# Optimization experiments

Hardware: AMD Instinct MI355X
Metric: run time of the kernel (lower is better)

## Reference

```python
import jax, jax.numpy as jnp
import numpy as np

N = 50000        # nodes
E = 800000       # edges
E_PAIR = 200000  # pos/neg link pairs
IN = 256
HID = (512, 256, 160)
NEG_SLOPE = 0.2


def _lin_w(k, i, o):
    s = 1.0 / np.sqrt(i)
    return jax.random.uniform(k, (i, o), jnp.float32, -s, s)


def setup_inputs() -> dict:
    key = jax.random.key(0)
    ks = jax.random.split(key, 16)
    inp = {
        'x': jax.random.normal(ks[0], (N, IN), jnp.float32),
        'w': jax.random.uniform(ks[1], (E,), jnp.float32),
        'src': jax.random.randint(ks[2], (E,), 0, N),
        'dst': jax.random.randint(ks[3], (E,), 0, N),
        'pos_src': jax.random.randint(ks[4], (E_PAIR,), 0, N),
        'pos_dst': jax.random.randint(ks[5], (E_PAIR,), 0, N),
        'neg_src': jax.random.randint(ks[6], (E_PAIR,), 0, N),
        'neg_dst': jax.random.randint(ks[7], (E_PAIR,), 0, N),
        # GraphConv weights/biases
        'W1': _lin_w(ks[8], IN, HID[0]), 'b1': jnp.zeros((HID[0],), jnp.float32),
        'W2': _lin_w(ks[9], HID[0], HID[1]), 'b2': jnp.zeros((HID[1],), jnp.float32),
        'W3': _lin_w(ks[10], HID[1], HID[2]), 'b3': jnp.zeros((HID[2],), jnp.float32),
        # predictor MLP: 160 -> 80 -> 40 -> 1
        'P1': _lin_w(ks[11], HID[2], HID[2] // 2), 'pb1': jnp.zeros((HID[2] // 2,), jnp.float32),
        'P2': _lin_w(ks[12], HID[2] // 2, HID[2] // 4), 'pb2': jnp.zeros((HID[2] // 4,), jnp.float32),
        'P3': _lin_w(ks[13], HID[2] // 4, 1), 'pb3': jnp.zeros((1,), jnp.float32),
    }
    return inp


def _degree_norms(src, dst):
    ones = jnp.ones((E,), jnp.float32)
    out_deg = jnp.clip(jax.ops.segment_sum(ones, src, num_segments=N), 1.0)
    in_deg = jnp.clip(jax.ops.segment_sum(ones, dst, num_segments=N), 1.0)
    # norm='both': D_out^{-1/2} on source side, D_in^{-1/2} on dest side
    return (out_deg ** -0.5)[:, None], (in_deg ** -0.5)[:, None]


def _graph_conv(h, W, b, src, dst, w, out_norm, in_norm, project_first):
    # DGL GraphConv (norm='both', edge_weight=w): scale src feats, multiply
    # messages by edge weight, sum-aggregate, scale by in-degree norm, + bias.
    # DGL projects before aggregation iff in_feats > out_feats (same math).
    h = h * out_norm
    if project_first:
        h = h @ W
    agg = jax.ops.segment_sum(h[src] * w[:, None], dst, num_segments=N)
    if not project_first:
        agg = agg @ W
    return agg * in_norm + b


def _predictor(z, P1, pb1, P2, pb2, P3, pb3):
    z = jax.nn.leaky_relu(z @ P1 + pb1, NEG_SLOPE)
    z = jax.nn.leaky_relu(z @ P2 + pb2, NEG_SLOPE)
    return z @ P3 + pb3


def reference(x, w, src, dst, pos_src, pos_dst, neg_src, neg_dst,
              W1, b1, W2, b2, W3, b3, P1, pb1, P2, pb2, P3, pb3):
    out_norm, in_norm = _degree_norms(src, dst)
    h = _graph_conv(x, W1, b1, src, dst, w, out_norm, in_norm, project_first=False)  # 256<=512
    h = jax.nn.relu(h)
    h = _graph_conv(h, W2, b2, src, dst, w, out_norm, in_norm, project_first=True)   # 512>256
    h = jax.nn.relu(h)
    h = _graph_conv(h, W3, b3, src, dst, w, out_norm, in_norm, project_first=True)   # 256>160
    h_pos = _predictor(h[pos_src] * h[pos_dst], P1, pb1, P2, pb2, P3, pb3)
    h_neg = _predictor(h[neg_src] * h[neg_dst], P1, pb1, P2, pb2, P3, pb3)
    return h_pos, h_neg, h
```

## Files before the change

kernel.cpp:

```cpp
#include <hip/hip_runtime.h>
#include <math.h>

#define NN 50000
#define EE 800000
#define NPAIR 200000

typedef unsigned short u16;
typedef short short8v __attribute__((ext_vector_type(8)));
typedef float float16v __attribute__((ext_vector_type(16)));

__device__ __forceinline__ float leaky(float x){ return x >= 0.f ? x : 0.2f*x; }

__device__ __forceinline__ u16 bfhi(float x){
  union{float f; unsigned u;} v; v.f = x;
  unsigned r = (v.u + 0x7FFFu + ((v.u >> 16) & 1u)) >> 16;
  return (u16)r;
}
__device__ __forceinline__ float bf2f(u16 h){
  union{unsigned u; float f;} v; v.u = ((unsigned)h) << 16; return v.f;
}
__device__ __forceinline__ void split2(float x, float y, unsigned &hp, unsigned &lp){
  u16 hx = bfhi(x), hy = bfhi(y);
  u16 lx = bfhi(x - bf2f(hx)), ly = bfhi(y - bf2f(hy));
  hp = (unsigned)hx | ((unsigned)hy << 16);
  lp = (unsigned)lx | ((unsigned)ly << 16);
}
#define MFMA_BF16 __builtin_amdgcn_mfma_f32_32x32x16_bf16


__global__ void degree_kernel(const int* __restrict__ src, const int* __restrict__ dst,
                              int* cnt_out, int* cnt_in){
  int i = blockIdx.x*blockDim.x + threadIdx.x;
  if(i < EE){
    atomicAdd(&cnt_out[src[i]], 1);
    atomicAdd(&cnt_in[dst[i]], 1);
  }
}

__global__ void norm_kernel(const int* __restrict__ cnt_out, const int* __restrict__ cnt_in,
                            float* __restrict__ out_norm, float* __restrict__ in_norm){
  int i = blockIdx.x*blockDim.x + threadIdx.x;
  if(i < NN){
    int o = cnt_out[i]; if(o < 1) o = 1;
    int d = cnt_in[i];  if(d < 1) d = 1;
    out_norm[i] = 1.f/sqrtf((float)o);
    in_norm[i]  = 1.f/sqrtf((float)d);
  }
}

__global__ void scan_kernel(const int* __restrict__ cnt, int* __restrict__ row_off){
  const int T = 512;
  __shared__ int sums[T];
  int t = threadIdx.x;
  int chunk = (NN + T - 1)/T;
  int base = t*chunk;
  int hi = base + chunk; if(hi > NN) hi = NN;
  int s = 0;
  for(int i = base; i < hi; i++) s += cnt[i];
  sums[t] = s;
  __syncthreads();
  for(int off = 1; off < T; off <<= 1){
    int add = (t >= off) ? sums[t-off] : 0;
    __syncthreads();
    sums[t] += add;
    __syncthreads();
  }
  int run = sums[t] - s;
  for(int i = base; i < hi; i++){ row_off[i] = run; run += cnt[i]; }
  if(t == T-1) row_off[NN] = EE;
}

__global__ void bucket_kernel(const int* __restrict__ src, const int* __restrict__ dst,
                              const float* __restrict__ w, const float* __restrict__ out_norm,
                              const int* __restrict__ row_off,
                              int* fill, int* __restrict__ es, float* __restrict__ ew){
  int i = blockIdx.x*blockDim.x + threadIdx.x;
  if(i < EE){
    int d = dst[i];
    int s = src[i];
    int p = row_off[d] + atomicAdd(&fill[d], 1);
    es[p] = s;
    ew[p] = w[i] * out_norm[s];
  }
}

__global__ void wsplit_kernel(const float* __restrict__ W, int K, int M,
                              u16* __restrict__ Whi, u16* __restrict__ Wlo){
  int i = blockIdx.x*256 + threadIdx.x;
  if(i < K*M){
    int m = i / K, k = i - m*K;
    float a = W[(size_t)k*M + m];
    u16 h = bfhi(a);
    Whi[i] = h;
    Wlo[i] = bfhi(a - bf2f(h));
  }
}

__global__ void psplit_kernel(const float* __restrict__ P1, const float* __restrict__ P2,
                              u16* __restrict__ P1th, u16* __restrict__ P1tl,
                              u16* __restrict__ P2th, u16* __restrict__ P2tl){
  int i = blockIdx.x*256 + threadIdx.x;
  if(i < 96*160){
    int c = i/160, k = i - c*160;
    float v = (c < 80) ? P1[k*80 + c] : 0.f;
    u16 h = bfhi(v);
    P1th[i] = h; P1tl[i] = bfhi(v - bf2f(h));
  }
  if(i < 64*80){
    int c = i/80, k = i - c*80;
    float v = (c < 40) ? P2[k*40 + c] : 0.f;
    u16 h = bfhi(v);
    P2th[i] = h; P2tl[i] = bfhi(v - bf2f(h));
  }
}

template<int F, int MODE>
__global__ __launch_bounds__(256) void agg_kernel(
    const float* __restrict__ feat, const int* __restrict__ es,
    const float* __restrict__ ew, const int* __restrict__ row_off,
    const float* __restrict__ innorm, const float* __restrict__ bias,
    float* __restrict__ out_f, u16* __restrict__ out_h, u16* __restrict__ out_l){
  constexpr int F4 = F/4;
  int wid = threadIdx.x >> 6, lane = threadIdx.x & 63;
  int v = blockIdx.x*4 + wid;
  if(v >= NN || lane >= F4) return;
  int s = row_off[v], e = row_off[v+1];
  const float4* f4 = (const float4*)feat;
  float4 a0 = {0,0,0,0}, a1 = {0,0,0,0}, a2 = {0,0,0,0}, a3 = {0,0,0,0};
  int j = s;
  for(; j + 7 < e; j += 8){
    int   i0 = es[j],   i1 = es[j+1], i2 = es[j+2], i3 = es[j+3];
    int   i4 = es[j+4], i5 = es[j+5], i6 = es[j+6], i7 = es[j+7];
    float w0 = ew[j],   w1 = ew[j+1], w2 = ew[j+2], w3 = ew[j+3];
    float w4 = ew[j+4], w5 = ew[j+5], w6 = ew[j+6], w7 = ew[j+7];
    float4 r0 = f4[(size_t)i0*F4 + lane];
    float4 r1 = f4[(size_t)i1*F4 + lane];
    float4 r2 = f4[(size_t)i2*F4 + lane];
    float4 r3 = f4[(size_t)i3*F4 + lane];
    float4 r4 = f4[(size_t)i4*F4 + lane];
    float4 r5 = f4[(size_t)i5*F4 + lane];
    float4 r6 = f4[(size_t)i6*F4 + lane];
    float4 r7 = f4[(size_t)i7*F4 + lane];
    a0.x += r0.x*w0; a0.y += r0.y*w0; a0.z += r0.z*w0; a0.w += r0.w*w0;
    a1.x += r1.x*w1; a1.y += r1.y*w1; a1.z += r1.z*w1; a1.w += r1.w*w1;
    a2.x += r2.x*w2; a2.y += r2.y*w2; a2.z += r2.z*w2; a2.w += r2.w*w2;
    a3.x += r3.x*w3; a3.y += r3.y*w3; a3.z += r3.z*w3; a3.w += r3.w*w3;
    a0.x += r4.x*w4; a0.y += r4.y*w4; a0.z += r4.z*w4; a0.w += r4.w*w4;
    a1.x += r5.x*w5; a1.y += r5.y*w5; a1.z += r5.z*w5; a1.w += r5.w*w5;
    a2.x += r6.x*w6; a2.y += r6.y*w6; a2.z += r6.z*w6; a2.w += r6.w*w6;
    a3.x += r7.x*w7; a3.y += r7.y*w7; a3.z += r7.z*w7; a3.w += r7.w*w7;
  }
  for(; j + 3 < e; j += 4){
    int   i0 = es[j],   i1 = es[j+1], i2 = es[j+2], i3 = es[j+3];
    float w0 = ew[j],   w1 = ew[j+1], w2 = ew[j+2], w3 = ew[j+3];
    float4 r0 = f4[(size_t)i0*F4 + lane];
    float4 r1 = f4[(size_t)i1*F4 + lane];
    float4 r2 = f4[(size_t)i2*F4 + lane];
    float4 r3 = f4[(size_t)i3*F4 + lane];
    a0.x += r0.x*w0; a0.y += r0.y*w0; a0.z += r0.z*w0; a0.w += r0.w*w0;
    a1.x += r1.x*w1; a1.y += r1.y*w1; a1.z += r1.z*w1; a1.w += r1.w*w1;
    a2.x += r2.x*w2; a2.y += r2.y*w2; a2.z += r2.z*w2; a2.w += r2.w*w2;
    a3.x += r3.x*w3; a3.y += r3.y*w3; a3.z += r3.z*w3; a3.w += r3.w*w3;
  }
  for(; j < e; j++){
    int idx = es[j]; float wt = ew[j];
    float4 r = f4[(size_t)idx*F4 + lane];
    a0.x += r.x*wt; a0.y += r.y*wt; a0.z += r.z*wt; a0.w += r.w*wt;
  }
  float4 r;
  r.x = (a0.x+a1.x)+(a2.x+a3.x);
  r.y = (a0.y+a1.y)+(a2.y+a3.y);
  r.z = (a0.z+a1.z)+(a2.z+a3.z);
  r.w = (a0.w+a1.w)+(a2.w+a3.w);
  if(MODE >= 1){
    float inm = innorm[v];
    float4 bb = *(const float4*)&bias[lane*4];
    r.x = r.x*inm + bb.x; r.y = r.y*inm + bb.y;
    r.z = r.z*inm + bb.z; r.w = r.w*inm + bb.w;
    if(MODE == 1){
      r.x = fmaxf(r.x, 0.f); r.y = fmaxf(r.y, 0.f);
      r.z = fmaxf(r.z, 0.f); r.w = fmaxf(r.w, 0.f);
    }
  }
  if(MODE == 2){
    ((float4*)(out_f + (size_t)v*F))[lane] = r;
  } else {
    unsigned hp0, lp0, hp1, lp1;
    split2(r.x, r.y, hp0, lp0);
    split2(r.z, r.w, hp1, lp1);
    *(uint2*)&out_h[(size_t)v*F + lane*4] = make_uint2(hp0, hp1);
    *(uint2*)&out_l[(size_t)v*F + lane*4] = make_uint2(lp0, lp1);
  }
}

template<int OM>
__global__ __launch_bounds__(256) void gemm_mfma(
    const u16* __restrict__ Ahi, const u16* __restrict__ Alo,
    const u16* __restrict__ Bhi, const u16* __restrict__ Blo,
    float* __restrict__ C, u16* __restrict__ Chi, u16* __restrict__ Clo,
    int K, int M,
    const float* __restrict__ innorm, const float* __restrict__ bias){
  __shared__ u16 sAhi[128*40];
  __shared__ u16 sAlo[128*40];
  __shared__ u16 sBhi[128*40];
  __shared__ u16 sBlo[128*40];
  int tid = threadIdx.x;
  int row0 = blockIdx.x*128, col0 = blockIdx.y*128;
  int wv = tid >> 6, L = tid & 63;
  int wr = (wv >> 1)*64, wc = (wv & 1)*64;
  int srow = tid >> 1, skh = (tid & 1)*16;

  float16v acc[2][2];
  #pragma unroll
  for(int i = 0; i < 2; i++)
    #pragma unroll
    for(int j = 0; j < 2; j++)
      #pragma unroll
      for(int r = 0; r < 16; r++) acc[i][j][r] = 0.f;

  bool av = (row0 + srow) < NN;
  bool bv = (col0 + srow) < M;
  const u16* ahsrc = Ahi + (size_t)(row0 + srow)*K;
  const u16* alsrc = Alo + (size_t)(row0 + srow)*K;
  const u16* bhsrc = Bhi + (size_t)(col0 + srow)*K;
  const u16* blsrc = Blo + (size_t)(col0 + srow)*K;
  const uint4 z4 = make_uint4(0,0,0,0);

  for(int k0 = 0; k0 < K; k0 += 32){
    uint4 ah0 = z4, ah1 = z4, al0 = z4, al1 = z4;
    if(av){
      ah0 = *(const uint4*)&ahsrc[k0 + skh];
      ah1 = *(const uint4*)&ahsrc[k0 + skh + 8];
      al0 = *(const uint4*)&alsrc[k0 + skh];
      al1 = *(const uint4*)&alsrc[k0 + skh + 8];
    }
    uint4 bh0 = z4, bh1 = z4, bl0 = z4, bl1 = z4;
    if(bv){
      bh0 = *(const uint4*)&bhsrc[k0 + skh];
      bh1 = *(const uint4*)&bhsrc[k0 + skh + 8];
      bl0 = *(const uint4*)&blsrc[k0 + skh];
      bl1 = *(const uint4*)&blsrc[k0 + skh + 8];
    }
    __syncthreads();
    int sa = srow*40 + skh;
    *(uint4*)&sAhi[sa]     = ah0;
    *(uint4*)&sAhi[sa + 8] = ah1;
    *(uint4*)&sAlo[sa]     = al0;
    *(uint4*)&sAlo[sa + 8] = al1;
    *(uint4*)&sBhi[sa]     = bh0;
    *(uint4*)&sBhi[sa + 8] = bh1;
    *(uint4*)&sBlo[sa]     = bl0;
    *(uint4*)&sBlo[sa + 8] = bl1;
    __syncthreads();
    #pragma unroll
    for(int ks = 0; ks < 2; ks++){
      int ko = ks*16 + (L >> 5)*8;
      int ra0 = (wr + (L & 31))*40 + ko, ra1 = ra0 + 32*40;
      int rb0 = (wc + (L & 31))*40 + ko, rb1 = rb0 + 32*40;
      short8v ah0v = *(const short8v*)&sAhi[ra0];
      short8v ah1v = *(const short8v*)&sAhi[ra1];
      short8v al0v = *(const short8v*)&sAlo[ra0];
      short8v al1v = *(const short8v*)&sAlo[ra1];
      short8v bhf0 = *(const short8v*)&sBhi[rb0];
      short8v bhf1 = *(const short8v*)&sBhi[rb1];
      short8v blf0 = *(const short8v*)&sBlo[rb0];
      short8v blf1 = *(const short8v*)&sBlo[rb1];
      acc[0][0] = MFMA_BF16(ah0v, bhf0, acc[0][0], 0,0,0);
      acc[0][0] = MFMA_BF16(al0v, bhf0, acc[0][0], 0,0,0);
      acc[0][0] = MFMA_BF16(ah0v, blf0, acc[0][0], 0,0,0);
      acc[0][1] = MFMA_BF16(ah0v, bhf1, acc[0][1], 0,0,0);
      acc[0][1] = MFMA_BF16(al0v, bhf1, acc[0][1], 0,0,0);
      acc[0][1] = MFMA_BF16(ah0v, blf1, acc[0][1], 0,0,0);
      acc[1][0] = MFMA_BF16(ah1v, bhf0, acc[1][0], 0,0,0);
      acc[1][0] = MFMA_BF16(al1v, bhf0, acc[1][0], 0,0,0);
      acc[1][0] = MFMA_BF16(ah1v, blf0, acc[1][0], 0,0,0);
      acc[1][1] = MFMA_BF16(ah1v, bhf1, acc[1][1], 0,0,0);
      acc[1][1] = MFMA_BF16(al1v, bhf1, acc[1][1], 0,0,0);
      acc[1][1] = MFMA_BF16(ah1v, blf1, acc[1][1], 0,0,0);
    }
  }

  int cB = L & 31, rq = 4*(L >> 5);
  #pragma unroll
  for(int tr = 0; tr < 2; tr++){
    #pragma unroll
    for(int tc = 0; tc < 2; tc++){
      int c = col0 + wc + tc*32 + cB;
      if(c >= M) continue;
      #pragma unroll
      for(int reg = 0; reg < 16; reg++){
        int r = row0 + wr + tr*32 + (reg & 3) + 8*(reg >> 2) + rq;
        if(r >= NN) continue;
        float v = acc[tr][tc][reg];
        if(OM == 0){
          C[(size_t)r*M + c] = v;
        } else {
          float t = fmaxf(v*innorm[r] + bias[c], 0.f);
          u16 h = bfhi(t);
          size_t idx = (size_t)r*M + c;
          Chi[idx] = h;
          Clo[idx] = bfhi(t - bf2f(h));
        }
      }
    }
  }
}

#define ZSTR 168
#define P1STR 24
#define Y1STR 88
__global__ __launch_bounds__(256) void predictor_mfma(
    const float* __restrict__ h3,
    const int* __restrict__ ps, const int* __restrict__ pd,
    const int* __restrict__ ns, const int* __restrict__ nd,
    const u16* __restrict__ P1th, const u16* __restrict__ P1tl,
    const float* __restrict__ pb1,
    const u16* __restrict__ P2th, const u16* __restrict__ P2tl,
    const float* __restrict__ pb2,
    const float* __restrict__ P3, const float* __restrict__ pb3,
    float* __restrict__ out){
  __shared__ u16 smem[26112];
  u16* zh  = smem;
  u16* zl  = smem + 64*ZSTR;
  u16* p1h = smem + 2*64*ZSTR;
  u16* p1l = p1h + 96*P1STR;
  u16* y1h = smem;
  u16* y1l = smem + 64*Y1STR;
  u16* p2h = smem + 2*64*Y1STR;
  u16* p2l = smem + 3*64*Y1STR;
  float* part = (float*)(smem + 4*64*Y1STR);

  int tid = threadIdx.x;
  int pair0 = blockIdx.x*64;
  int w = tid >> 6, L = tid & 63;
  int lrow = L & 31, lk = (L >> 5)*8;

  {
    int p = tid >> 2, sub = tid & 3;
    int q = pair0 + p;
    int a, b;
    if(q < NPAIR){ a = ps[q]; b = pd[q]; }
    else         { a = ns[q-NPAIR]; b = nd[q-NPAIR]; }
    const float4* ra = (const float4*)(h3 + (size_t)a*160);
    const float4* rb = (const float4*)(h3 + (size_t)b*160);
    #pragma unroll
    for(int it = 0; it < 10; it++){
      int g = sub + it*4;
      float4 va = ra[g], vb = rb[g];
      unsigned hp0, lp0, hp1, lp1;
      split2(va.x*vb.x, va.y*vb.y, hp0, lp0);
      split2(va.z*vb.z, va.w*vb.w, hp1, lp1);
      *(uint2*)&zh[p*ZSTR + 4*g] = make_uint2(hp0, hp1);
      *(uint2*)&zl[p*ZSTR + 4*g] = make_uint2(lp0, lp1);
    }
  }

  float16v acc1a, acc1b;
  #pragma unroll
  for(int r = 0; r < 16; r++){ acc1a[r] = 0.f; acc1b[r] = 0.f; }
  int j1 = w, j2 = (w < 2) ? (w + 4) : -1;
  int pt1 = j1/3, ct1 = j1 - pt1*3;
  int pt2 = (j2 >= 0) ? j2/3 : 0;
  int ct2j = (j2 >= 0) ? (j2 - pt2*3) : 0;

  for(int k0 = 0; k0 < 160; k0 += 16){
    __syncthreads();
    if(tid < 192){
      int c = tid >> 1, half = tid & 1;
      uint4 vh = *(const uint4*)&P1th[c*160 + k0 + half*8];
      uint4 vl = *(const uint4*)&P1tl[c*160 + k0 + half*8];
      *(uint4*)&p1h[c*P1STR + half*8] = vh;
      *(uint4*)&p1l[c*P1STR + half*8] = vl;
    }
    __syncthreads();
    {
      short8v ah = *(const short8v*)&zh[(pt1*32 + lrow)*ZSTR + k0 + lk];
      short8v al = *(const short8v*)&zl[(pt1*32 + lrow)*ZSTR + k0 + lk];
      short8v bh = *(const short8v*)&p1h[(ct1*32 + lrow)*P1STR + lk];
      short8v bl = *(const short8v*)&p1l[(ct1*32 + lrow)*P1STR + lk];
      acc1a = MFMA_BF16(ah, bh, acc1a, 0,0,0);
      acc1a = MFMA_BF16(al, bh, acc1a, 0,0,0);
      acc1a = MFMA_BF16(ah, bl, acc1a, 0,0,0);
    }
    if(j2 >= 0){
      short8v ah = *(const short8v*)&zh[(pt2*32 + lrow)*ZSTR + k0 + lk];
      short8v al = *(const short8v*)&zl[(pt2*32 + lrow)*ZSTR + k0 + lk];
      short8v bh = *(const short8v*)&p1h[(ct2j*32 + lrow)*P1STR + lk];
      short8v bl = *(const short8v*)&p1l[(ct2j*32 + lrow)*P1STR + lk];
      acc1b = MFMA_BF16(ah, bh, acc1b, 0,0,0);
      acc1b = MFMA_BF16(al, bh, acc1b, 0,0,0);
      acc1b = MFMA_BF16(ah, bl, acc1b, 0,0,0);
    }
  }
  __syncthreads();

  {
    int c = ct1*32 + lrow;
    if(c < 80){
      float pb = pb1[c];
      #pragma unroll
      for(int r = 0; r < 16; r++){
        int p = pt1*32 + (r & 3) + 8*(r >> 2) + 4*(L >> 5);
        float v = leaky(acc1a[r] + pb);
        u16 h = bfhi(v);
        y1h[p*Y1STR + c] = h;
        y1l[p*Y1STR + c] = bfhi(v - bf2f(h));
      }
    }
  }
  if(j2 >= 0){
    int c = ct2j*32 + lrow;
    if(c < 80){
      float pb = pb1[c];
      #pragma unroll
      for(int r = 0; r < 16; r++){
        int p = pt2*32 + (r & 3) + 8*(r >> 2) + 4*(L >> 5);
        float v = leaky(acc1b[r] + pb);
        u16 h = bfhi(v);
        y1h[p*Y1STR + c] = h;
        y1l[p*Y1STR + c] = bfhi(v - bf2f(h));
      }
    }
  }
  for(int i = tid; i < 640; i += 256){
    int c = i/10, jj = i - c*10;
    *(uint4*)&p2h[c*Y1STR + jj*8] = *(const uint4*)&P2th[c*80 + jj*8];
    *(uint4*)&p2l[c*Y1STR + jj*8] = *(const uint4*)&P2tl[c*80 + jj*8];
  }
  __syncthreads();

  float16v acc2;
  #pragma unroll
  for(int r = 0; r < 16; r++) acc2[r] = 0.f;
  int pt = w & 1, c2t = w >> 1;
  for(int k0 = 0; k0 < 80; k0 += 16){
    short8v ah = *(const short8v*)&y1h[(pt*32 + lrow)*Y1STR + k0 + lk];
    short8v al = *(const short8v*)&y1l[(pt*32 + lrow)*Y1STR + k0 + lk];
    short8v bh = *(const short8v*)&p2h[(c2t*32 + lrow)*Y1STR + k0 + lk];
    short8v bl = *(const short8v*)&p2l[(c2t*32 + lrow)*Y1STR + k0 + lk];
    acc2 = MFMA_BF16(ah, bh, acc2, 0,0,0);
    acc2 = MFMA_BF16(al, bh, acc2, 0,0,0);
    acc2 = MFMA_BF16(ah, bl, acc2, 0,0,0);
  }

  int c2 = c2t*32 + lrow;
  float pb2c = (c2 < 40) ? pb2[c2] : 0.f;
  float p3c  = (c2 < 40) ? P3[c2]  : 0.f;
  float vals[16];
  #pragma unroll
  for(int r = 0; r < 16; r++){
    float v = leaky(acc2[r] + pb2c) * p3c;
    #pragma unroll
    for(int m = 1; m < 32; m <<= 1) v += __shfl_xor(v, m);
    vals[r] = v;
  }
  if(lrow == 0){
    #pragma unroll
    for(int r = 0; r < 16; r++){
      int p = pt*32 + (r & 3) + 8*(r >> 2) + 4*(L >> 5);
      part[c2t*64 + p] = vals[r];
    }
  }
  __syncthreads();
  if(tid < 64) out[pair0 + tid] = (part[tid] + part[64 + tid]) + pb3[0];
}


extern "C" void kernel_launch(void* const* d_in, const int* in_sizes, int n_in,
                              void* d_out, int out_size, void* d_ws, size_t ws_size,
                              hipStream_t stream) {
  const float* x  = (const float*)d_in[0];
  const float* w  = (const float*)d_in[1];
  const int* src  = (const int*)d_in[2];
  const int* dst  = (const int*)d_in[3];
  const int* ps   = (const int*)d_in[4];
  const int* pd   = (const int*)d_in[5];
  const int* ns   = (const int*)d_in[6];
  const int* nd   = (const int*)d_in[7];
  const float* W1 = (const float*)d_in[8];  const float* b1  = (const float*)d_in[9];
  const float* W2 = (const float*)d_in[10]; const float* b2  = (const float*)d_in[11];
  const float* W3 = (const float*)d_in[12]; const float* b3  = (const float*)d_in[13];
  const float* P1 = (const float*)d_in[14]; const float* pb1 = (const float*)d_in[15];
  const float* P2 = (const float*)d_in[16]; const float* pb2 = (const float*)d_in[17];
  const float* P3 = (const float*)d_in[18]; const float* pb3 = (const float*)d_in[19];
  float* out = (float*)d_out;

  char* p = (char*)d_ws;
  auto alloc = [&](size_t bytes)->char*{
    char* r = p; p += (bytes + 255) & ~(size_t)255; return r;
  };
  int*   cnt_out = (int*)  alloc(NN*4);
  int*   cnt_in  = (int*)  alloc(NN*4);
  int*   fill    = (int*)  alloc(NN*4);
  int*   row_off = (int*)  alloc((NN+1)*4);
  float* out_nrm = (float*)alloc(NN*4);
  float* in_nrm  = (float*)alloc(NN*4);
  int*   es      = (int*)  alloc((size_t)EE*4);
  float* ew      = (float*)alloc((size_t)EE*4);
  u16*   w1h     = (u16*)  alloc(256*512*2);
  u16*   w1l     = (u16*)  alloc(256*512*2);
  u16*   w2h     = (u16*)  alloc(512*256*2);
  u16*   w2l     = (u16*)  alloc(512*256*2);
  u16*   w3h     = (u16*)  alloc(256*160*2);
  u16*   w3l     = (u16*)  alloc(256*160*2);
  u16*   p1th    = (u16*)  alloc(96*160*2);
  u16*   p1tl    = (u16*)  alloc(96*160*2);
  u16*   p2th    = (u16*)  alloc(64*80*2);
  u16*   p2tl    = (u16*)  alloc(64*80*2);
  u16*   ch      = (u16*)  alloc((size_t)NN*256*2);
  u16*   cl      = (u16*)  alloc((size_t)NN*256*2);
  u16*   h1h     = (u16*)  alloc((size_t)NN*512*2);
  u16*   h1l     = (u16*)  alloc((size_t)NN*512*2);
  float* bufB    = (float*)alloc((size_t)NN*256*4);

  size_t cntPad = (NN*4 + 255) & ~(size_t)255;
  hipMemsetAsync(cnt_out, 0, 3*cntPad, stream);

  degree_kernel<<<(EE+255)/256, 256, 0, stream>>>(src, dst, cnt_out, cnt_in);
  norm_kernel<<<(NN+255)/256, 256, 0, stream>>>(cnt_out, cnt_in, out_nrm, in_nrm);
  scan_kernel<<<1, 512, 0, stream>>>(cnt_in, row_off);
  bucket_kernel<<<(EE+255)/256, 256, 0, stream>>>(src, dst, w, out_nrm, row_off, fill, es, ew);
  wsplit_kernel<<<512, 256, 0, stream>>>(W1, 256, 512, w1h, w1l);
  wsplit_kernel<<<512, 256, 0, stream>>>(W2, 512, 256, w2h, w2l);
  wsplit_kernel<<<160, 256, 0, stream>>>(W3, 256, 160, w3h, w3l);
  psplit_kernel<<<60, 256, 0, stream>>>(P1, P2, p1th, p1tl, p2th, p2tl);

  int aggGrid = (NN + 3)/4;

  agg_kernel<256,0><<<aggGrid, 256, 0, stream>>>(x, es, ew, row_off, nullptr, nullptr,
                                                 nullptr, ch, cl);
  gemm_mfma<1><<<dim3(391,4), 256, 0, stream>>>(ch, cl, w1h, w1l,
                                                nullptr, h1h, h1l, 256, 512, in_nrm, b1);

  gemm_mfma<0><<<dim3(391,2), 256, 0, stream>>>(h1h, h1l, w2h, w2l,
                                                bufB, nullptr, nullptr, 512, 256, nullptr, nullptr);
  agg_kernel<256,1><<<aggGrid, 256, 0, stream>>>(bufB, es, ew, row_off, in_nrm, b2,
                                                 nullptr, ch, cl);

  gemm_mfma<0><<<dim3(391,2), 256, 0, stream>>>(ch, cl, w3h, w3l,
                                                bufB, nullptr, nullptr, 256, 160, nullptr, nullptr);
  agg_kernel<160,2><<<aggGrid, 256, 0, stream>>>(bufB, es, ew, row_off, in_nrm, b3,
                                                 out + 2*NPAIR, nullptr, nullptr);

  predictor_mfma<<<(2*NPAIR)/64, 256, 0, stream>>>(out + 2*NPAIR, ps, pd, ns, nd,
                                                   p1th, p1tl, pb1, p2th, p2tl, pb2,
                                                   P3, pb3, out);
}
```

Baseline: 947.9 us.

## Interleave hi/lo bf16 split operands in swizzled blocks and load GEMM tiles via global_load_lds

Changes the storage of the split-bf16 activations and weights from separate hi and lo arrays to one interleaved, XOR-swizzled layout. Each 32-wide k-block of a row holds hi and lo chunks together. The producers (wsplit, agg, the gemm epilogue) write this layout, and the GEMM stages tiles straight from global memory into LDS with global_load_lds instead of going through registers. The goal is to cut register traffic and LDS bank conflicts in the GEMM mainloop. In exchange the GEMM depends on padded row buffers (NNP) and no longer bounds-checks rows and columns. The scan kernel also moves to 1024 threads with vectorised int4 loads.

```diff
diff --git a/kernel.cpp b/kernel.cpp
--- a/kernel.cpp
+++ b/kernel.cpp
@@ -2,6 +2,7 @@
 #include <math.h>
 
 #define NN 50000
+#define NNP 50048
 #define EE 800000
 #define NPAIR 200000
 
@@ -26,6 +27,13 @@
   lp = (unsigned)lx | ((unsigned)ly << 16);
 }
 #define MFMA_BF16 __builtin_amdgcn_mfma_f32_32x32x16_bf16
+
+__device__ __forceinline__ void gload16(const u16* g, u16* l){
+  __builtin_amdgcn_global_load_lds(
+      (const __attribute__((address_space(1))) unsigned int*)(g),
+      (__attribute__((address_space(3))) unsigned int*)(l), 16, 0, 0);
+}
+
 
 
 __global__ void degree_kernel(const int* __restrict__ src, const int* __restrict__ dst,
@@ -49,14 +57,21 @@
 }
 
 __global__ void scan_kernel(const int* __restrict__ cnt, int* __restrict__ row_off){
-  const int T = 512;
+  const int T = 1024;
+  const int CH = 52;
   __shared__ int sums[T];
   int t = threadIdx.x;
-  int chunk = (NN + T - 1)/T;
-  int base = t*chunk;
-  int hi = base + chunk; if(hi > NN) hi = NN;
+  int base = t*CH;
+  int hi = base + CH; if(hi > NN) hi = NN;
   int s = 0;
-  for(int i = base; i < hi; i++) s += cnt[i];
+  if(base < NN){
+    int i = base;
+    for(; i + 3 < hi; i += 4){
+      int4 v = *(const int4*)&cnt[i];
+      s += (v.x + v.y) + (v.z + v.w);
+    }
+    for(; i < hi; i++) s += cnt[i];
+  }
   sums[t] = s;
   __syncthreads();
   for(int off = 1; off < T; off <<= 1){
@@ -66,7 +81,9 @@
     __syncthreads();
   }
   int run = sums[t] - s;
-  for(int i = base; i < hi; i++){ row_off[i] = run; run += cnt[i]; }
+  if(base < NN){
+    for(int i = base; i < hi; i++){ row_off[i] = run; run += cnt[i]; }
+  }
   if(t == T-1) row_off[NN] = EE;
 }
 
@@ -85,14 +102,17 @@
 }
 
 __global__ void wsplit_kernel(const float* __restrict__ W, int K, int M,
-                              u16* __restrict__ Whi, u16* __restrict__ Wlo){
+                              u16* __restrict__ PS){
   int i = blockIdx.x*256 + threadIdx.x;
   if(i < K*M){
     int m = i / K, k = i - m*K;
     float a = W[(size_t)k*M + m];
     u16 h = bfhi(a);
-    Whi[i] = h;
-    Wlo[i] = bfhi(a - bf2f(h));
+    u16 lo = bfhi(a - bf2f(h));
+    int kb = k >> 5, j = k & 31, c = j >> 3, swz = m & 7;
+    size_t base = ((size_t)m*(K >> 5) + kb)*64 + (j & 7);
+    PS[base + ((c    ) ^ swz)*8] = h;
+    PS[base + ((c + 4) ^ swz)*8] = lo;
   }
 }
 
@@ -119,7 +139,7 @@
     const float* __restrict__ feat, const int* __restrict__ es,
     const float* __restrict__ ew, const int* __restrict__ row_off,
     const float* __restrict__ innorm, const float* __restrict__ bias,
-    float* __restrict__ out_f, u16* __restrict__ out_h, u16* __restrict__ out_l){
+    float* __restrict__ out_f, u16* __restrict__ out_ps){
   constexpr int F4 = F/4;
   int wid = threadIdx.x >> 6, lane = threadIdx.x & 63;
   int v = blockIdx.x*4 + wid;
@@ -188,27 +208,26 @@
     unsigned hp0, lp0, hp1, lp1;
     split2(r.x, r.y, hp0, lp0);
     split2(r.z, r.w, hp1, lp1);
-    *(uint2*)&out_h[(size_t)v*F + lane*4] = make_uint2(hp0, hp1);
-    *(uint2*)&out_l[(size_t)v*F + lane*4] = make_uint2(lp0, lp1);
+    int kb = lane >> 3, ch = (lane >> 1) & 3, swz = v & 7, off = (lane & 1)*4;
+    u16* row = out_ps + ((size_t)v*(F >> 5) + kb)*64;
+    *(uint2*)&row[((ch    ) ^ swz)*8 + off] = make_uint2(hp0, hp1);
+    *(uint2*)&row[((ch + 4) ^ swz)*8 + off] = make_uint2(lp0, lp1);
   }
 }
 
 template<int OM>
 __global__ __launch_bounds__(256) void gemm_mfma(
-    const u16* __restrict__ Ahi, const u16* __restrict__ Alo,
-    const u16* __restrict__ Bhi, const u16* __restrict__ Blo,
-    float* __restrict__ C, u16* __restrict__ Chi, u16* __restrict__ Clo,
+    const u16* __restrict__ APS, const u16* __restrict__ BPS,
+    float* __restrict__ C, u16* __restrict__ CPS,
     int K, int M,
     const float* __restrict__ innorm, const float* __restrict__ bias){
-  __shared__ u16 sAhi[128*40];
-  __shared__ u16 sAlo[128*40];
-  __shared__ u16 sBhi[128*40];
-  __shared__ u16 sBlo[128*40];
+  __shared__ u16 sA[8192];
+  __shared__ u16 sB[8192];
   int tid = threadIdx.x;
   int row0 = blockIdx.x*128, col0 = blockIdx.y*128;
   int wv = tid >> 6, L = tid & 63;
   int wr = (wv >> 1)*64, wc = (wv & 1)*64;
-  int srow = tid >> 1, skh = (tid & 1)*16;
+  int KB = K >> 5;
 
   float16v acc[2][2];
   #pragma unroll
@@ -218,65 +237,47 @@
       #pragma unroll
       for(int r = 0; r < 16; r++) acc[i][j][r] = 0.f;
 
-  bool av = (row0 + srow) < NN;
-  bool bv = (col0 + srow) < M;
-  const u16* ahsrc = Ahi + (size_t)(row0 + srow)*K;
-  const u16* alsrc = Alo + (size_t)(row0 + srow)*K;
-  const u16* bhsrc = Bhi + (size_t)(col0 + srow)*K;
-  const u16* blsrc = Blo + (size_t)(col0 + srow)*K;
-  const uint4 z4 = make_uint4(0,0,0,0);
-
-  for(int k0 = 0; k0 < K; k0 += 32){
-    uint4 ah0 = z4, ah1 = z4, al0 = z4, al1 = z4;
-    if(av){
-      ah0 = *(const uint4*)&ahsrc[k0 + skh];
-      ah1 = *(const uint4*)&ahsrc[k0 + skh + 8];
-      al0 = *(const uint4*)&alsrc[k0 + skh];
-      al1 = *(const uint4*)&alsrc[k0 + skh + 8];
-    }
-    uint4 bh0 = z4, bh1 = z4, bl0 = z4, bl1 = z4;
-    if(bv){
-      bh0 = *(const uint4*)&bhsrc[k0 + skh];
-      bh1 = *(const uint4*)&bhsrc[k0 + skh + 8];
-      bl0 = *(const uint4*)&blsrc[k0 + skh];
-      bl1 = *(const uint4*)&blsrc[k0 + skh + 8];
-    }
+  const u16* abase = APS + (size_t)row0*KB*64;
+  const u16* bbase = BPS + (size_t)col0*KB*64;
+  int lr8 = L >> 3, lc8 = (L & 7)*8;
+
+  for(int kblk = 0; kblk < KB; kblk++){
     __syncthreads();
-    int sa = srow*40 + skh;
-    *(uint4*)&sAhi[sa]     = ah0;
-    *(uint4*)&sAhi[sa + 8] = ah1;
-    *(uint4*)&sAlo[sa]     = al0;
-    *(uint4*)&sAlo[sa + 8] = al1;
-    *(uint4*)&sBhi[sa]     = bh0;
-    *(uint4*)&sBhi[sa + 8] = bh1;
-    *(uint4*)&sBlo[sa]     = bl0;
-    *(uint4*)&sBlo[sa + 8] = bl1;
+    #pragma unroll
+    for(int i = 0; i < 4; i++){
+      int rb = wv*32 + i*8;
+      gload16(abase + ((size_t)(rb + lr8)*KB + kblk)*64 + lc8, &sA[rb*64]);
+      gload16(bbase + ((size_t)(rb + lr8)*KB + kblk)*64 + lc8, &sB[rb*64]);
+    }
     __syncthreads();
     #pragma unroll
     for(int ks = 0; ks < 2; ks++){
-      int ko = ks*16 + (L >> 5)*8;
-      int ra0 = (wr + (L & 31))*40 + ko, ra1 = ra0 + 32*40;
-      int rb0 = (wc + (L & 31))*40 + ko, rb1 = rb0 + 32*40;
-      short8v ah0v = *(const short8v*)&sAhi[ra0];
-      short8v ah1v = *(const short8v*)&sAhi[ra1];
-      short8v al0v = *(const short8v*)&sAlo[ra0];
-      short8v al1v = *(const short8v*)&sAlo[ra1];
-      short8v bhf0 = *(const short8v*)&sBhi[rb0];
-      short8v bhf1 = *(const short8v*)&sBhi[rb1];
-      short8v blf0 = *(const short8v*)&sBlo[rb0];
-      short8v blf1 = *(const short8v*)&sBlo[rb1];
-      acc[0][0] = MFMA_BF16(ah0v, bhf0, acc[0][0], 0,0,0);
-      acc[0][0] = MFMA_BF16(al0v, bhf0, acc[0][0], 0,0,0);
-      acc[0][0] = MFMA_BF16(ah0v, blf0, acc[0][0], 0,0,0);
-      acc[0][1] = MFMA_BF16(ah0v, bhf1, acc[0][1], 0,0,0);
-      acc[0][1] = MFMA_BF16(al0v, bhf1, acc[0][1], 0,0,0);
-      acc[0][1] = MFMA_BF16(ah0v, blf1, acc[0][1], 0,0,0);
-      acc[1][0] = MFMA_BF16(ah1v, bhf0, acc[1][0], 0,0,0);
-      acc[1][0] = MFMA_BF16(al1v, bhf0, acc[1][0], 0,0,0);
-      acc[1][0] = MFMA_BF16(ah1v, blf0, acc[1][0], 0,0,0);
-      acc[1][1] = MFMA_BF16(ah1v, bhf1, acc[1][1], 0,0,0);
-      acc[1][1] = MFMA_BF16(al1v, bhf1, acc[1][1], 0,0,0);
-      acc[1][1] = MFMA_BF16(ah1v, blf1, acc[1][1], 0,0,0);
+      int swz = L & 7;
+      int ch = ks*2 + (L >> 5);
+      int oh = ((ch    ) ^ swz)*8;
+      int ol = ((ch + 4) ^ swz)*8;
+      int r0 = (wr + (L & 31))*64, r1 = r0 + 32*64;
+      int q0 = (wc + (L & 31))*64, q1 = q0 + 32*64;
+      short8v ah0 = *(const short8v*)&sA[r0 + oh];
+      short8v al0 = *(const short8v*)&sA[r0 + ol];
+      short8v ah1 = *(const short8v*)&sA[r1 + oh];
+      short8v al1 = *(const short8v*)&sA[r1 + ol];
+      short8v bh0 = *(const short8v*)&sB[q0 + oh];
+      short8v bl0 = *(const short8v*)&sB[q0 + ol];
+      short8v bh1 = *(const short8v*)&sB[q1 + oh];
+      short8v bl1 = *(const short8v*)&sB[q1 + ol];
+      acc[0][0] = MFMA_BF16(ah0, bh0, acc[0][0], 0,0,0);
+      acc[0][0] = MFMA_BF16(al0, bh0, acc[0][0], 0,0,0);
+      acc[0][0] = MFMA_BF16(ah0, bl0, acc[0][0], 0,0,0);
+      acc[0][1] = MFMA_BF16(ah0, bh1, acc[0][1], 0,0,0);
+      acc[0][1] = MFMA_BF16(al0, bh1, acc[0][1], 0,0,0);
+      acc[0][1] = MFMA_BF16(ah0, bl1, acc[0][1], 0,0,0);
+      acc[1][0] = MFMA_BF16(ah1, bh0, acc[1][0], 0,0,0);
+      acc[1][0] = MFMA_BF16(al1, bh0, acc[1][0], 0,0,0);
+      acc[1][0] = MFMA_BF16(ah1, bl0, acc[1][0], 0,0,0);
+      acc[1][1] = MFMA_BF16(ah1, bh1, acc[1][1], 0,0,0);
+      acc[1][1] = MFMA_BF16(al1, bh1, acc[1][1], 0,0,0);
+      acc[1][1] = MFMA_BF16(ah1, bl1, acc[1][1], 0,0,0);
     }
   }
 
@@ -297,9 +298,11 @@
         } else {
           float t = fmaxf(v*innorm[r] + bias[c], 0.f);
           u16 h = bfhi(t);
-          size_t idx = (size_t)r*M + c;
-          Chi[idx] = h;
-          Clo[idx] = bfhi(t - bf2f(h));
+          u16 lo = bfhi(t - bf2f(h));
+          int kb = c >> 5, jj = c & 31, cc = jj >> 3, swz = r & 7;
+          size_t base = ((size_t)r*(M >> 5) + kb)*64 + (jj & 7);
+          CPS[base + ((cc    ) ^ swz)*8] = h;
+          CPS[base + ((cc + 4) ^ swz)*8] = lo;
         }
       }
     }
@@ -497,20 +500,15 @@
   float* in_nrm  = (float*)alloc(NN*4);
   int*   es      = (int*)  alloc((size_t)EE*4);
   float* ew      = (float*)alloc((size_t)EE*4);
-  u16*   w1h     = (u16*)  alloc(256*512*2);
-  u16*   w1l     = (u16*)  alloc(256*512*2);
-  u16*   w2h     = (u16*)  alloc(512*256*2);
-  u16*   w2l     = (u16*)  alloc(512*256*2);
-  u16*   w3h     = (u16*)  alloc(256*160*2);
-  u16*   w3l     = (u16*)  alloc(256*160*2);
+  u16*   w1PS    = (u16*)  alloc((size_t)512*512*2);
+  u16*   w2PS    = (u16*)  alloc((size_t)256*1024*2);
+  u16*   w3PS    = (u16*)  alloc((size_t)256*512*2);
   u16*   p1th    = (u16*)  alloc(96*160*2);
   u16*   p1tl    = (u16*)  alloc(96*160*2);
   u16*   p2th    = (u16*)  alloc(64*80*2);
   u16*   p2tl    = (u16*)  alloc(64*80*2);
-  u16*   ch      = (u16*)  alloc((size_t)NN*256*2);
-  u16*   cl      = (u16*)  alloc((size_t)NN*256*2);
-  u16*   h1h     = (u16*)  alloc((size_t)NN*512*2);
-  u16*   h1l     = (u16*)  alloc((size_t)NN*512*2);
+  u16*   aggPS   = (u16*)  alloc((size_t)NNP*512*2);
+  u16*   h1PS    = (u16*)  alloc((size_t)NNP*1024*2);
   float* bufB    = (float*)alloc((size_t)NN*256*4);
 
   size_t cntPad = (NN*4 + 255) & ~(size_t)255;
@@ -518,29 +516,29 @@
 
   degree_kernel<<<(EE+255)/256, 256, 0, stream>>>(src, dst, cnt_out, cnt_in);
   norm_kernel<<<(NN+255)/256, 256, 0, stream>>>(cnt_out, cnt_in, out_nrm, in_nrm);
-  scan_kernel<<<1, 512, 0, stream>>>(cnt_in, row_off);
+  scan_kernel<<<1, 1024, 0, stream>>>(cnt_in, row_off);
   bucket_kernel<<<(EE+255)/256, 256, 0, stream>>>(src, dst, w, out_nrm, row_off, fill, es, ew);
-  wsplit_kernel<<<512, 256, 0, stream>>>(W1, 256, 512, w1h, w1l);
-  wsplit_kernel<<<512, 256, 0, stream>>>(W2, 512, 256, w2h, w2l);
-  wsplit_kernel<<<160, 256, 0, stream>>>(W3, 256, 160, w3h, w3l);
+  wsplit_kernel<<<512, 256, 0, stream>>>(W1, 256, 512, w1PS);
+  wsplit_kernel<<<512, 256, 0, stream>>>(W2, 512, 256, w2PS);
+  wsplit_kernel<<<160, 256, 0, stream>>>(W3, 256, 160, w3PS);
   psplit_kernel<<<60, 256, 0, stream>>>(P1, P2, p1th, p1tl, p2th, p2tl);
 
   int aggGrid = (NN + 3)/4;
 
   agg_kernel<256,0><<<aggGrid, 256, 0, stream>>>(x, es, ew, row_off, nullptr, nullptr,
-                                                 nullptr, ch, cl);
-  gemm_mfma<1><<<dim3(391,4), 256, 0, stream>>>(ch, cl, w1h, w1l,
-                                                nullptr, h1h, h1l, 256, 512, in_nrm, b1);
-
-  gemm_mfma<0><<<dim3(391,2), 256, 0, stream>>>(h1h, h1l, w2h, w2l,
-                                                bufB, nullptr, nullptr, 512, 256, nullptr, nullptr);
+                                                 nullptr, aggPS);
+  gemm_mfma<1><<<dim3(391,4), 256, 0, stream>>>(aggPS, w1PS, nullptr, h1PS,
+                                                256, 512, in_nrm, b1);
+
+  gemm_mfma<0><<<dim3(391,2), 256, 0, stream>>>(h1PS, w2PS, bufB, nullptr,
+                                                512, 256, nullptr, nullptr);
   agg_kernel<256,1><<<aggGrid, 256, 0, stream>>>(bufB, es, ew, row_off, in_nrm, b2,
-                                                 nullptr, ch, cl);
-
-  gemm_mfma<0><<<dim3(391,2), 256, 0, stream>>>(ch, cl, w3h, w3l,
-                                                bufB, nullptr, nullptr, 256, 160, nullptr, nullptr);
+                                                 nullptr, aggPS);
+
+  gemm_mfma<0><<<dim3(391,2), 256, 0, stream>>>(aggPS, w3PS, bufB, nullptr,
+                                                256, 160, nullptr, nullptr);
   agg_kernel<160,2><<<aggGrid, 256, 0, stream>>>(bufB, es, ew, row_off, in_nrm, b3,
-                                                 out + 2*NPAIR, nullptr, nullptr);
+                                                 out + 2*NPAIR, nullptr);
 
   predictor_mfma<<<(2*NPAIR)/64, 256, 0, stream>>>(out + 2*NPAIR, ps, pd, ns, nd,
                                                    p1th, p1tl, pb1, p2th, p2tl, pb2,
```

Result: faster. 902.3 us (-4.8%).
